# Optimization experiments

Measured on AMD Instinct MI355X. Metric: run time of the kernel, lower is better.

## Reference

```python
import jax, jax.numpy as jnp
import numpy as np

INPUT_DIM = 128
DEPTH = 6
HIDDEN = 64
NUM_INNER = 2 ** DEPTH - 1  # 63
NUM_LEAVES = 2 ** DEPTH     # 64


def setup_inputs() -> dict:
    key = jax.random.key(0)
    ks = jax.random.split(key, 6)
    x = jax.random.normal(ks[0], (65536, INPUT_DIM), dtype=jnp.float32)
    s1 = 1.0 / np.sqrt(INPUT_DIM)
    s2 = 1.0 / np.sqrt(HIDDEN)
    W1 = jax.random.uniform(ks[1], (NUM_INNER, INPUT_DIM, HIDDEN), minval=-s1, maxval=s1, dtype=jnp.float32)
    b1 = jax.random.uniform(ks[2], (NUM_INNER, HIDDEN), minval=-s1, maxval=s1, dtype=jnp.float32)
    W2 = jax.random.uniform(ks[3], (NUM_INNER, HIDDEN), minval=-s2, maxval=s2, dtype=jnp.float32)
    b2 = jax.random.uniform(ks[4], (NUM_INNER,), minval=-s2, maxval=s2, dtype=jnp.float32)
    leaf = jax.random.normal(ks[5], (NUM_LEAVES, 1), dtype=jnp.float32)
    return {"x": x, "W1": W1, "b1": b1, "W2": W2, "b2": b2, "leaf": leaf}


def reference(x, W1, b1, W2, b2, leaf):
    # All inner-node MLPs as one batched GEMM pair: [B, N] node probabilities
    h = jax.nn.relu(jnp.einsum('bi,nih->bnh', x, W1) + b1)      # [B, N, H]
    probs = jax.nn.sigmoid(jnp.einsum('bnh,nh->bn', h, W2) + b2)  # [B, N]

    # Original code walks node_idx = 2*node_idx+1 unconditionally, so the chain
    # of used node indices is 2^k - 1 for k = 0..depth-1.
    chain = jnp.array([2 ** k - 1 for k in range(DEPTH)], dtype=jnp.int32)
    p_chain = probs[:, chain]  # [B, D]

    # Bit k (LSB first) of leaf index selects p (bit=1) vs 1-p (bit=0)
    leaves = np.arange(NUM_LEAVES)
    bits = jnp.asarray(((leaves[:, None] >> np.arange(DEPTH)[None, :]) & 1).astype(np.float32))  # [L, D]

    # path_probs[b, l] = prod_k ( bits[l,k]*p + (1-bits[l,k])*(1-p) )
    factors = bits[None, :, :] * p_chain[:, None, :] + (1.0 - bits[None, :, :]) * (1.0 - p_chain[:, None, :])  # [B, L, D]
    path_probs = jnp.prod(factors, axis=-1)  # [B, L]

    return (path_probs @ leaf)[:, 0]  # [B]
```

## Files before the change

### kernel.cpp

```cpp
#include <hip/hip_runtime.h>

typedef __attribute__((ext_vector_type(4))) float f32x4;
typedef __attribute__((ext_vector_type(8))) short bf16x8;
typedef __attribute__((ext_vector_type(4))) unsigned int u32x4;

#define IDIM   128
#define HID    64
#define TDEPTH 6
#define MTILE  64
#define NWAVES 6
#define BLOCK  (NWAVES * 64)

__device__ __forceinline__ unsigned short f2bf(float f) {
    unsigned int u = __builtin_bit_cast(unsigned int, f);
    unsigned int r = (u + 0x7FFFu + ((u >> 16) & 1u)) >> 16;
    return (unsigned short)r;
}

__device__ __forceinline__ unsigned int f2bf_pk(float f0, float f1) {
    unsigned int u0 = __builtin_bit_cast(unsigned int, f0);
    unsigned int u1 = __builtin_bit_cast(unsigned int, f1);
    unsigned int t0 = u0 + 0x7FFFu + ((u0 >> 16) & 1u);
    unsigned int t1 = u1 + 0x7FFFu + ((u1 >> 16) & 1u);
    return (t1 & 0xFFFF0000u) | (t0 >> 16);
}

__global__ __launch_bounds__(BLOCK, 2)
void sdt_kernel(const float* __restrict__ x, const float* __restrict__ W1,
                const float* __restrict__ b1, const float* __restrict__ W2,
                const float* __restrict__ b2, const float* __restrict__ leaf,
                float* __restrict__ out) {
    __shared__ unsigned short xs[MTILE][IDIM + 8];
    __shared__ float p_lds[TDEPTH][MTILE];
    __shared__ float pp[4][MTILE];

    const int tid    = threadIdx.x;
    const int m_base = blockIdx.x * MTILE;

    const float4* xv = reinterpret_cast<const float4*>(x) + (size_t)m_base * (IDIM / 4);
    for (int f = tid; f < MTILE * (IDIM / 4); f += BLOCK) {
        int row = f >> 5;
        int c4  = f & 31;
        float4 v = xv[row * 32 + c4];
        unsigned long long pk =
            (unsigned long long)f2bf(v.x) |
            ((unsigned long long)f2bf(v.y) << 16) |
            ((unsigned long long)f2bf(v.z) << 32) |
            ((unsigned long long)f2bf(v.w) << 48);
        *reinterpret_cast<unsigned long long*>(&xs[row][c4 * 4]) = pk;
    }

    const int wave = tid >> 6;
    const int lane = tid & 63;
    const int node = (1 << wave) - 1;
    const int lcol = lane & 15;
    const int lq   = lane >> 4;

    float b1v[4], w2v[4];
    #pragma unroll
    for (int ct = 0; ct < 4; ct++) {
        int col = ct * 16 + lcol;
        b1v[ct] = b1[node * HID + col];
        w2v[ct] = W2[node * HID + col];
    }
    const float bias2 = b2[node];

    __syncthreads();

    f32x4 acc[4][4];
    #pragma unroll
    for (int rt = 0; rt < 4; rt++)
        #pragma unroll
        for (int ct = 0; ct < 4; ct++)
            acc[rt][ct] = (f32x4){0.f, 0.f, 0.f, 0.f};

    const float* wsrc = W1 + (size_t)node * IDIM * HID + lcol;
    #pragma unroll
    for (int ks = 0; ks < 4; ks++) {
        const int k0 = ks * 32 + lq * 8;
        bf16x8 bfrag[4];
        #pragma unroll
        for (int ct = 0; ct < 4; ct++) {
            const float* wc = wsrc + (size_t)k0 * HID + ct * 16;
            u32x4 pk;
            #pragma unroll
            for (int jp = 0; jp < 4; jp++)
                pk[jp] = f2bf_pk(wc[(2 * jp) * HID], wc[(2 * jp + 1) * HID]);
            bfrag[ct] = __builtin_bit_cast(bf16x8, pk);
        }
        bf16x8 afrag[4];
        #pragma unroll
        for (int rt = 0; rt < 4; rt++)
            afrag[rt] = *reinterpret_cast<const bf16x8*>(&xs[rt * 16 + lcol][ks * 32 + lq * 8]);
        #pragma unroll
        for (int rt = 0; rt < 4; rt++)
            #pragma unroll
            for (int ct = 0; ct < 4; ct++)
                acc[rt][ct] = __builtin_amdgcn_mfma_f32_16x16x32_bf16(
                    afrag[rt], bfrag[ct], acc[rt][ct], 0, 0, 0);
    }

    #pragma unroll
    for (int rt = 0; rt < 4; rt++) {
        #pragma unroll
        for (int r = 0; r < 4; r++) {
            float s = 0.f;
            #pragma unroll
            for (int ct = 0; ct < 4; ct++) {
                float v = acc[rt][ct][r] + b1v[ct];
                v = v > 0.f ? v : 0.f;
                s += v * w2v[ct];
            }
            #pragma unroll
            for (int d = 1; d < 16; d <<= 1)
                s += __shfl_xor(s, d, 64);
            float p = 1.f / (1.f + __expf(-(s + bias2)));
            if (lcol == 0)
                p_lds[wave][rt * 16 + lq * 4 + r] = p;
        }
    }
    __syncthreads();

    if (tid < 4 * MTILE) {
        int row = tid & (MTILE - 1);
        int ch  = tid >> 6;
        float q0 = p_lds[0][row];
        float q1 = p_lds[1][row];
        float q2 = p_lds[2][row];
        float q3 = p_lds[3][row];
        float p4 = p_lds[4][row];
        float p5 = p_lds[5][row];
        float f4 = (ch & 1) ? p4 : 1.f - p4;
        float f5 = (ch & 2) ? p5 : 1.f - p5;
        const float* lf = leaf + ch * 16;
        float t[8];
        #pragma unroll
        for (int j = 0; j < 8; j++) {
            float a = lf[2 * j], b = lf[2 * j + 1];
            t[j] = a + q0 * (b - a);
        }
        #pragma unroll
        for (int j = 0; j < 4; j++) t[j] = t[2 * j] + q1 * (t[2 * j + 1] - t[2 * j]);
        #pragma unroll
        for (int j = 0; j < 2; j++) t[j] = t[2 * j] + q2 * (t[2 * j + 1] - t[2 * j]);
        float s = t[0] + q3 * (t[1] - t[0]);
        pp[ch][row] = f4 * f5 * s;
    }
    __syncthreads();
    if (tid < MTILE)
        out[m_base + tid] = (pp[0][tid] + pp[1][tid]) + (pp[2][tid] + pp[3][tid]);
}

extern "C" void kernel_launch(void* const* d_in, const int* in_sizes, int n_in,
                              void* d_out, int out_size, void* d_ws, size_t ws_size,
                              hipStream_t stream) {
    const float* x    = (const float*)d_in[0];
    const float* W1   = (const float*)d_in[1];
    const float* b1   = (const float*)d_in[2];
    const float* W2   = (const float*)d_in[3];
    const float* b2   = (const float*)d_in[4];
    const float* leaf = (const float*)d_in[5];
    float* out = (float*)d_out;

    const int Bn = in_sizes[0] / IDIM;
    const int nblocks = Bn / MTILE;

    (void)d_ws; (void)ws_size;
    sdt_kernel<<<nblocks, BLOCK, 0, stream>>>(x, W1, b1, W2, b2, leaf, out);
}
```

Baseline: 112.4 us.

## Make blocks persistent over four tiles with register-prefetched double-buffered x

Each block now handles four 64-row tiles instead of one. The W1 weights are converted to bf16 fragments once per block and kept in registers, so this cost is amortised across the tiles. The next x tile is prefetched into registers while the current tile runs its MFMAs, then written into a second LDS buffer, overlapping global loads with compute. This cuts the grid to 256 blocks and raises register pressure (64 extra VGPRs for bfrag plus the prefetch registers), which may reduce occupancy and parallelism across the device.

```diff
diff --git a/kernel.cpp b/kernel.cpp
--- a/kernel.cpp
+++ b/kernel.cpp
@@ -4,12 +4,13 @@
 typedef __attribute__((ext_vector_type(8))) short bf16x8;
 typedef __attribute__((ext_vector_type(4))) unsigned int u32x4;
 
-#define IDIM   128
-#define HID    64
-#define TDEPTH 6
-#define MTILE  64
-#define NWAVES 6
-#define BLOCK  (NWAVES * 64)
+#define IDIM    128
+#define HID     64
+#define TDEPTH  6
+#define MTILE   64
+#define NWAVES  6
+#define BLOCK   (NWAVES * 64)
+#define T_TILES 4
 
 __device__ __forceinline__ unsigned short f2bf(float f) {
     unsigned int u = __builtin_bit_cast(unsigned int, f);
@@ -30,31 +31,46 @@
                 const float* __restrict__ b1, const float* __restrict__ W2,
                 const float* __restrict__ b2, const float* __restrict__ leaf,
                 float* __restrict__ out) {
-    __shared__ unsigned short xs[MTILE][IDIM + 8];
+    __shared__ unsigned short xs[2][MTILE][IDIM + 8];
     __shared__ float p_lds[TDEPTH][MTILE];
     __shared__ float pp[4][MTILE];
 
-    const int tid    = threadIdx.x;
-    const int m_base = blockIdx.x * MTILE;
-
-    const float4* xv = reinterpret_cast<const float4*>(x) + (size_t)m_base * (IDIM / 4);
-    for (int f = tid; f < MTILE * (IDIM / 4); f += BLOCK) {
-        int row = f >> 5;
-        int c4  = f & 31;
-        float4 v = xv[row * 32 + c4];
-        unsigned long long pk =
-            (unsigned long long)f2bf(v.x) |
-            ((unsigned long long)f2bf(v.y) << 16) |
-            ((unsigned long long)f2bf(v.z) << 32) |
-            ((unsigned long long)f2bf(v.w) << 48);
-        *reinterpret_cast<unsigned long long*>(&xs[row][c4 * 4]) = pk;
-    }
+    const int tid   = threadIdx.x;
+    const int tile0 = blockIdx.x * T_TILES;
 
     const int wave = tid >> 6;
     const int lane = tid & 63;
     const int node = (1 << wave) - 1;
     const int lcol = lane & 15;
     const int lq   = lane >> 4;
+
+    const float4* xv = reinterpret_cast<const float4*>(x);
+
+    float4 sreg[6];
+    {
+        const float4* xt = xv + (size_t)tile0 * (MTILE * IDIM / 4);
+        #pragma unroll
+        for (int i = 0; i < 5; i++) sreg[i] = xt[tid + i * BLOCK];
+        if (tid < 128) sreg[5] = xt[5 * BLOCK + tid];
+    }
+
+    bf16x8 bfrag[4][4];
+    {
+        const float* wsrc = W1 + (size_t)node * IDIM * HID + lcol;
+        #pragma unroll
+        for (int ks = 0; ks < 4; ks++) {
+            const int k0 = ks * 32 + lq * 8;
+            #pragma unroll
+            for (int ct = 0; ct < 4; ct++) {
+                const float* wc = wsrc + (size_t)k0 * HID + ct * 16;
+                u32x4 pk;
+                #pragma unroll
+                for (int jp = 0; jp < 4; jp++)
+                    pk[jp] = f2bf_pk(wc[(2 * jp) * HID], wc[(2 * jp + 1) * HID]);
+                bfrag[ks][ct] = __builtin_bit_cast(bf16x8, pk);
+            }
+        }
+    }
 
     float b1v[4], w2v[4];
     #pragma unroll
@@ -65,90 +81,136 @@
     }
     const float bias2 = b2[node];
 
+    #pragma unroll
+    for (int i = 0; i < 5; i++) {
+        int f = tid + i * BLOCK, row = f >> 5, c4 = f & 31;
+        float4 v = sreg[i];
+        unsigned long long pk =
+            (unsigned long long)f2bf(v.x) |
+            ((unsigned long long)f2bf(v.y) << 16) |
+            ((unsigned long long)f2bf(v.z) << 32) |
+            ((unsigned long long)f2bf(v.w) << 48);
+        *reinterpret_cast<unsigned long long*>(&xs[0][row][c4 * 4]) = pk;
+    }
+    if (tid < 128) {
+        int f = 5 * BLOCK + tid, row = f >> 5, c4 = f & 31;
+        float4 v = sreg[5];
+        unsigned long long pk =
+            (unsigned long long)f2bf(v.x) |
+            ((unsigned long long)f2bf(v.y) << 16) |
+            ((unsigned long long)f2bf(v.z) << 32) |
+            ((unsigned long long)f2bf(v.w) << 48);
+        *reinterpret_cast<unsigned long long*>(&xs[0][row][c4 * 4]) = pk;
+    }
     __syncthreads();
 
-    f32x4 acc[4][4];
-    #pragma unroll
-    for (int rt = 0; rt < 4; rt++)
-        #pragma unroll
-        for (int ct = 0; ct < 4; ct++)
-            acc[rt][ct] = (f32x4){0.f, 0.f, 0.f, 0.f};
-
-    const float* wsrc = W1 + (size_t)node * IDIM * HID + lcol;
-    #pragma unroll
-    for (int ks = 0; ks < 4; ks++) {
-        const int k0 = ks * 32 + lq * 8;
-        bf16x8 bfrag[4];
-        #pragma unroll
-        for (int ct = 0; ct < 4; ct++) {
-            const float* wc = wsrc + (size_t)k0 * HID + ct * 16;
-            u32x4 pk;
-            #pragma unroll
-            for (int jp = 0; jp < 4; jp++)
-                pk[jp] = f2bf_pk(wc[(2 * jp) * HID], wc[(2 * jp + 1) * HID]);
-            bfrag[ct] = __builtin_bit_cast(bf16x8, pk);
-        }
-        bf16x8 afrag[4];
+    int cur = 0;
+    for (int t = 0; t < T_TILES; ++t) {
+        const bool pf = (t + 1 < T_TILES);
+        if (pf) {
+            const float4* xt = xv + (size_t)(tile0 + t + 1) * (MTILE * IDIM / 4);
+            #pragma unroll
+            for (int i = 0; i < 5; i++) sreg[i] = xt[tid + i * BLOCK];
+            if (tid < 128) sreg[5] = xt[5 * BLOCK + tid];
+        }
+
+        f32x4 acc[4][4];
         #pragma unroll
         for (int rt = 0; rt < 4; rt++)
-            afrag[rt] = *reinterpret_cast<const bf16x8*>(&xs[rt * 16 + lcol][ks * 32 + lq * 8]);
-        #pragma unroll
-        for (int rt = 0; rt < 4; rt++)
             #pragma unroll
             for (int ct = 0; ct < 4; ct++)
-                acc[rt][ct] = __builtin_amdgcn_mfma_f32_16x16x32_bf16(
-                    afrag[rt], bfrag[ct], acc[rt][ct], 0, 0, 0);
-    }
-
-    #pragma unroll
-    for (int rt = 0; rt < 4; rt++) {
-        #pragma unroll
-        for (int r = 0; r < 4; r++) {
-            float s = 0.f;
-            #pragma unroll
-            for (int ct = 0; ct < 4; ct++) {
-                float v = acc[rt][ct][r] + b1v[ct];
-                v = v > 0.f ? v : 0.f;
-                s += v * w2v[ct];
-            }
-            #pragma unroll
-            for (int d = 1; d < 16; d <<= 1)
-                s += __shfl_xor(s, d, 64);
-            float p = 1.f / (1.f + __expf(-(s + bias2)));
-            if (lcol == 0)
-                p_lds[wave][rt * 16 + lq * 4 + r] = p;
-        }
-    }
-    __syncthreads();
-
-    if (tid < 4 * MTILE) {
-        int row = tid & (MTILE - 1);
-        int ch  = tid >> 6;
-        float q0 = p_lds[0][row];
-        float q1 = p_lds[1][row];
-        float q2 = p_lds[2][row];
-        float q3 = p_lds[3][row];
-        float p4 = p_lds[4][row];
-        float p5 = p_lds[5][row];
-        float f4 = (ch & 1) ? p4 : 1.f - p4;
-        float f5 = (ch & 2) ? p5 : 1.f - p5;
-        const float* lf = leaf + ch * 16;
-        float t[8];
-        #pragma unroll
-        for (int j = 0; j < 8; j++) {
-            float a = lf[2 * j], b = lf[2 * j + 1];
-            t[j] = a + q0 * (b - a);
-        }
-        #pragma unroll
-        for (int j = 0; j < 4; j++) t[j] = t[2 * j] + q1 * (t[2 * j + 1] - t[2 * j]);
-        #pragma unroll
-        for (int j = 0; j < 2; j++) t[j] = t[2 * j] + q2 * (t[2 * j + 1] - t[2 * j]);
-        float s = t[0] + q3 * (t[1] - t[0]);
-        pp[ch][row] = f4 * f5 * s;
-    }
-    __syncthreads();
-    if (tid < MTILE)
-        out[m_base + tid] = (pp[0][tid] + pp[1][tid]) + (pp[2][tid] + pp[3][tid]);
+                acc[rt][ct] = (f32x4){0.f, 0.f, 0.f, 0.f};
+        #pragma unroll
+        for (int ks = 0; ks < 4; ks++) {
+            bf16x8 afrag[4];
+            #pragma unroll
+            for (int rt = 0; rt < 4; rt++)
+                afrag[rt] = *reinterpret_cast<const bf16x8*>(
+                    &xs[cur][rt * 16 + lcol][ks * 32 + lq * 8]);
+            #pragma unroll
+            for (int rt = 0; rt < 4; rt++)
+                #pragma unroll
+                for (int ct = 0; ct < 4; ct++)
+                    acc[rt][ct] = __builtin_amdgcn_mfma_f32_16x16x32_bf16(
+                        afrag[rt], bfrag[ks][ct], acc[rt][ct], 0, 0, 0);
+        }
+
+        #pragma unroll
+        for (int rt = 0; rt < 4; rt++) {
+            #pragma unroll
+            for (int r = 0; r < 4; r++) {
+                float s = 0.f;
+                #pragma unroll
+                for (int ct = 0; ct < 4; ct++) {
+                    float v = acc[rt][ct][r] + b1v[ct];
+                    v = v > 0.f ? v : 0.f;
+                    s += v * w2v[ct];
+                }
+                #pragma unroll
+                for (int d = 1; d < 16; d <<= 1)
+                    s += __shfl_xor(s, d, 64);
+                float p = 1.f / (1.f + __expf(-(s + bias2)));
+                if (lcol == 0)
+                    p_lds[wave][rt * 16 + lq * 4 + r] = p;
+            }
+        }
+        __syncthreads();
+
+        if (pf) {
+            #pragma unroll
+            for (int i = 0; i < 5; i++) {
+                int f = tid + i * BLOCK, row = f >> 5, c4 = f & 31;
+                float4 v = sreg[i];
+                unsigned long long pk =
+                    (unsigned long long)f2bf(v.x) |
+                    ((unsigned long long)f2bf(v.y) << 16) |
+                    ((unsigned long long)f2bf(v.z) << 32) |
+                    ((unsigned long long)f2bf(v.w) << 48);
+                *reinterpret_cast<unsigned long long*>(&xs[cur ^ 1][row][c4 * 4]) = pk;
+            }
+            if (tid < 128) {
+                int f = 5 * BLOCK + tid, row = f >> 5, c4 = f & 31;
+                float4 v = sreg[5];
+                unsigned long long pk =
+                    (unsigned long long)f2bf(v.x) |
+                    ((unsigned long long)f2bf(v.y) << 16) |
+                    ((unsigned long long)f2bf(v.z) << 32) |
+                    ((unsigned long long)f2bf(v.w) << 48);
+                *reinterpret_cast<unsigned long long*>(&xs[cur ^ 1][row][c4 * 4]) = pk;
+            }
+        }
+
+        if (tid < 4 * MTILE) {
+            int row = tid & (MTILE - 1);
+            int ch  = tid >> 6;
+            float q0 = p_lds[0][row];
+            float q1 = p_lds[1][row];
+            float q2 = p_lds[2][row];
+            float q3 = p_lds[3][row];
+            float p4 = p_lds[4][row];
+            float p5 = p_lds[5][row];
+            float f4 = (ch & 1) ? p4 : 1.f - p4;
+            float f5 = (ch & 2) ? p5 : 1.f - p5;
+            const float* lf = leaf + ch * 16;
+            float tt[8];
+            #pragma unroll
+            for (int j = 0; j < 8; j++) {
+                float a = lf[2 * j], b = lf[2 * j + 1];
+                tt[j] = a + q0 * (b - a);
+            }
+            #pragma unroll
+            for (int j = 0; j < 4; j++) tt[j] = tt[2 * j] + q1 * (tt[2 * j + 1] - tt[2 * j]);
+            #pragma unroll
+            for (int j = 0; j < 2; j++) tt[j] = tt[2 * j] + q2 * (tt[2 * j + 1] - tt[2 * j]);
+            float s = tt[0] + q3 * (tt[1] - tt[0]);
+            pp[ch][row] = f4 * f5 * s;
+        }
+        __syncthreads();
+        if (tid < MTILE)
+            out[(size_t)(tile0 + t) * MTILE + tid] =
+                (pp[0][tid] + pp[1][tid]) + (pp[2][tid] + pp[3][tid]);
+        cur ^= 1;
+    }
 }
 
 extern "C" void kernel_launch(void* const* d_in, const int* in_sizes, int n_in,
@@ -163,7 +225,7 @@
     float* out = (float*)d_out;
 
     const int Bn = in_sizes[0] / IDIM;
-    const int nblocks = Bn / MTILE;
+    const int nblocks = Bn / (MTILE * T_TILES);
 
     (void)d_ws; (void)ws_size;
     sdt_kernel<<<nblocks, BLOCK, 0, stream>>>(x, W1, b1, W2, b2, leaf, out);
```

Measured after the change: 100.8 us. 10.3% less time.
